# Kernel optimization log

Hardware: AMD Instinct MI355X
Metric: run time of the kernel (lower is better)

Reference implementation:

```python
import jax, jax.numpy as jnp
import numpy as np

N_CLASSES = 8  # hardcoded by the (-1, 8, 8) reshape in the original layer

def setup_inputs() -> dict:
    key = jax.random.key(0)
    k1, k2, k3, k4 = jax.random.split(key, 4)
    B, F, C, R = 16384, 128, N_CLASSES, 64
    x = jax.random.normal(k1, (B, F), dtype=jnp.float32)
    p = jax.random.uniform(k2, (B, C), dtype=jnp.float32)  # class-prob-like input
    W = jax.random.normal(k3, (F, C * C, R), dtype=jnp.float32) * 0.02
    b = jax.random.normal(k4, (C, C, R), dtype=jnp.float32) * 0.1
    return {"x": x, "p": p, "W": W, "b": b}

def reference(x, p, W, b):
    # x: (B, 128) features; p: (B, C) class probs; W: (128, C*C, R); b: (C, C, R)
    B = x.shape[0]
    C = b.shape[0]
    R = b.shape[-1]
    # per-annotator GEMM fused across all annotators: (B, C*C, R)
    logits = jnp.einsum('bf,fkr->bkr', x, W).reshape(B, C, C, R) + b[None]
    # row-softmax: softmax over the "predicted class" axis for each true class c
    M = jax.nn.softmax(logits, axis=2)  # (B, C, C, R)
    # batched dot: p (B,C) contracted against rows of each annotator matrix
    out = jnp.einsum('bc,bcdr->bdr', p, M)  # (B, C, R)
    # NOTE: original applies K.dropout(0.5) (training-mode); omitted for a
    # deterministic inference reference (identity at eval).
    return out
```

## Files before the change

kernel.cpp:

```cpp
#include <hip/hip_runtime.h>
#include <hip/hip_bf16.h>


#define B_ROWS   16384
#define F_DIM    128
#define NCOL     4096
#define OUT_STRIDE 512
#define LOG2E    1.44269504088896340736f

typedef __bf16 bf16x8 __attribute__((ext_vector_type(8)));
typedef float  f32x4  __attribute__((ext_vector_type(4)));

#define AS1(p) ((const __attribute__((address_space(1))) unsigned int*)(p))
#define AS3(p) ((__attribute__((address_space(3))) unsigned int*)(p))

template <int CTRL>
__device__ __forceinline__ float dpp_add(float s) {
    int si = __builtin_bit_cast(int, s);
    int pi = __builtin_amdgcn_update_dpp(0, si, CTRL, 0xf, 0xf, true);
    return s + __builtin_bit_cast(float, pi);
}

__device__ __forceinline__ float swz4(float v) {
    return __builtin_bit_cast(float,
        __builtin_amdgcn_ds_swizzle(__builtin_bit_cast(int, v), 0x101F));
}


__global__ void wconv_kernel(const float* __restrict__ W, __bf16* __restrict__ wf) {
    int f    = blockIdx.x * 256 + threadIdx.x;
    int lane = f & 63;
    int tkk  = f >> 6;
    int T    = tkk >> 2;
    int kk   = tkk & 3;
    int c    = T >> 5;
    int w    = (T >> 3) & 3;
    int i    = T & 7;
    int col4 = lane & 15;
    int d    = (col4 & 3) | ((col4 >> 1) & 4);
    int r    = w * 16 + i * 2 + ((col4 >> 2) & 1);
    int n    = (c * 8 + d) * 64 + r;
    int kbase = kk * 32 + (lane >> 4) * 8;
    bf16x8 frag;
    for (int j = 0; j < 8; ++j)
        frag[j] = (__bf16)W[(kbase + j) * NCOL + n];
    *(bf16x8*)(wf + f * 8) = frag;
}

__global__ void bconv_kernel(const float* __restrict__ bias, float* __restrict__ bs) {
    int t    = blockIdx.x * 256 + threadIdx.x;
    int lane = t & 63;
    int T    = t >> 6;
    int c    = T >> 5;
    int w    = (T >> 3) & 3;
    int i    = T & 7;
    int col4 = lane & 15;
    int d    = (col4 & 3) | ((col4 >> 1) & 4);
    int r    = w * 16 + i * 2 + ((col4 >> 2) & 1);
    bs[t] = bias[(c * 8 + d) * 64 + r] * LOG2E;
}

__global__ __launch_bounds__(256, 2)
void fused_kernel(const float* __restrict__ x, const float* __restrict__ p,
                  const float* __restrict__ bs, const __bf16* __restrict__ wf,
                  float* __restrict__ out) {
    __shared__ __align__(16) char lds[2][32768];

    const int lane = threadIdx.x & 63;
    const int ww   = threadIdx.x >> 6;
    const int quad = lane >> 4;
    const int l15  = lane & 15;
    const int w    = blockIdx.x & 3;
    const int b0   = (blockIdx.x >> 2) * 128 + ww * 32;
    const int d    = (l15 & 3) | ((l15 >> 1) & 4);
    const int rb   = (l15 >> 2) & 1;

    bf16x8 afr[2][4];
#pragma unroll
    for (int mt = 0; mt < 2; ++mt) {
        const float* xr = x + (b0 + mt * 16 + l15) * F_DIM + quad * 8;
#pragma unroll
        for (int kk = 0; kk < 4; ++kk) {
            float4 lo = *(const float4*)(xr + kk * 32);
            float4 hi = *(const float4*)(xr + kk * 32 + 4);
            bf16x8 f;
            f[0] = (__bf16)lo.x; f[1] = (__bf16)lo.y;
            f[2] = (__bf16)lo.z; f[3] = (__bf16)lo.w;
            f[4] = (__bf16)hi.x; f[5] = (__bf16)hi.y;
            f[6] = (__bf16)hi.z; f[7] = (__bf16)hi.w;
            afr[mt][kk] = f;
        }
    }

    auto stage = [&](int c, char* dst) {
        const __bf16* gbase = wf + (size_t)(c * 128 + w * 32) * 512 + lane * 8;
#pragma unroll
        for (int j = 0; j < 8; ++j) {
            int f = ww * 8 + j;
            __builtin_amdgcn_global_load_lds(AS1(gbase + f * 512),
                                             AS3(dst + f * 1024), 16, 0, 0);
        }
    };

    float O_all[2][8][4] = {};

    stage(0, lds[0]);

#pragma unroll 1
    for (int c = 0; c < 8; ++c) {
        __syncthreads();
        if (c < 7) stage(c + 1, lds[(c + 1) & 1]);
        const char* buf = lds[c & 1];

        float pvv[2][4];
#pragma unroll
        for (int mt = 0; mt < 2; ++mt)
#pragma unroll
            for (int jj = 0; jj < 4; ++jj)
                pvv[mt][jj] = p[(b0 + mt * 16 + quad * 4 + jj) * 8 + c];

#pragma unroll
        for (int i = 0; i < 8; ++i) {
            bf16x8 bfr[4];
#pragma unroll
            for (int kk = 0; kk < 4; ++kk)
                bfr[kk] = *(const bf16x8*)(buf + (i * 4 + kk) * 1024 + lane * 16);
            f32x4 acc0 = {0.f, 0.f, 0.f, 0.f};
            f32x4 acc1 = {0.f, 0.f, 0.f, 0.f};
#pragma unroll
            for (int kk = 0; kk < 4; ++kk) {
                acc0 = __builtin_amdgcn_mfma_f32_16x16x32_bf16(afr[0][kk], bfr[kk], acc0, 0, 0, 0);
                acc1 = __builtin_amdgcn_mfma_f32_16x16x32_bf16(afr[1][kk], bfr[kk], acc1, 0, 0, 0);
            }
            float bvl = bs[(c * 32 + w * 8 + i) * 64 + lane];
#pragma unroll
            for (int mt = 0; mt < 2; ++mt) {
                const f32x4& acc = mt ? acc1 : acc0;
#pragma unroll
                for (int jj = 0; jj < 4; ++jj) {
                    float e = __builtin_amdgcn_exp2f(
                                  __builtin_fmaf(acc[jj], LOG2E, bvl));
                    float s = dpp_add<0xB1>(e);
                    s = dpp_add<0x4E>(s);
                    s = dpp_add<0x128>(s);
                    O_all[mt][i][jj] = __builtin_fmaf(
                        e, pvv[mt][jj] * __builtin_amdgcn_rcpf(s), O_all[mt][i][jj]);
                }
            }
        }
    }

    const bool bhi = (rb != 0);
#pragma unroll
    for (int mt = 0; mt < 2; ++mt) {
#pragma unroll
        for (int jj = 0; jj < 4; ++jj) {
            float S[8];
#pragma unroll
            for (int i = 0; i < 8; ++i)
                S[i] = swz4(O_all[mt][i][jj]);
            float T[8];
#pragma unroll
            for (int m = 0; m < 8; ++m) {
                int ilo = m >> 1, ihi = 4 + (m >> 1);
                float tlo = (m & 1) ? S[ilo]             : O_all[mt][ilo][jj];
                float thi = (m & 1) ? O_all[mt][ihi][jj] : S[ihi];
                T[m] = bhi ? thi : tlo;
            }
            float* orow = out + (b0 + mt * 16 + quad * 4 + jj) * OUT_STRIDE
                              + d * 64 + w * 16 + rb * 8;
            f32x4 v0 = {T[0], T[1], T[2], T[3]};
            f32x4 v1 = {T[4], T[5], T[6], T[7]};
            *(f32x4*)(orow)     = v0;
            *(f32x4*)(orow + 4) = v1;
        }
    }
}

extern "C" void kernel_launch(void* const* d_in, const int* in_sizes, int n_in,
                              void* d_out, int out_size, void* d_ws, size_t ws_size,
                              hipStream_t stream) {
    const float* x    = (const float*)d_in[0];
    const float* p    = (const float*)d_in[1];
    const float* W    = (const float*)d_in[2];
    const float* bias = (const float*)d_in[3];
    float* out = (float*)d_out;
    __bf16* wf = (__bf16*)d_ws;
    float*  bs = (float*)((char*)d_ws + (1 << 20));

    wconv_kernel<<<dim3(256), dim3(256), 0, stream>>>(W, wf);
    bconv_kernel<<<dim3(64), dim3(256), 0, stream>>>(bias, bs);
    fused_kernel<<<dim3(512), dim3(256), 0, stream>>>(x, p, bs, wf, out);
}
```

Baseline: 114.4 us.

## Split each block's columns across two wave halves with 512-thread blocks

Doubles the block size to eight waves, with each group of four waves handling half of the per-class column tiles for the same rows. This halves accumulator registers per thread and spreads the MFMA/softmax work over more waves to raise latency hiding. The cost is duplicated x fragment loads and p loads per wave pair, and a narrower output store per lane.

```diff
diff --git a/kernel.cpp b/kernel.cpp
--- a/kernel.cpp
+++ b/kernel.cpp
@@ -60,7 +60,7 @@
     bs[t] = bias[(c * 8 + d) * 64 + r] * LOG2E;
 }
 
-__global__ __launch_bounds__(256, 2)
+__global__ __launch_bounds__(512, 4)
 void fused_kernel(const float* __restrict__ x, const float* __restrict__ p,
                   const float* __restrict__ bs, const __bf16* __restrict__ wf,
                   float* __restrict__ out) {
@@ -68,10 +68,12 @@
 
     const int lane = threadIdx.x & 63;
     const int ww   = threadIdx.x >> 6;
+    const int mtp  = ww & 3;
+    const int h    = ww >> 2;
     const int quad = lane >> 4;
     const int l15  = lane & 15;
     const int w    = blockIdx.x & 3;
-    const int b0   = (blockIdx.x >> 2) * 128 + ww * 32;
+    const int b0   = (blockIdx.x >> 2) * 128 + mtp * 32;
     const int d    = (l15 & 3) | ((l15 >> 1) & 4);
     const int rb   = (l15 >> 2) & 1;
 
@@ -95,14 +97,14 @@
     auto stage = [&](int c, char* dst) {
         const __bf16* gbase = wf + (size_t)(c * 128 + w * 32) * 512 + lane * 8;
 #pragma unroll
-        for (int j = 0; j < 8; ++j) {
-            int f = ww * 8 + j;
+        for (int j = 0; j < 4; ++j) {
+            int f = ww * 4 + j;
             __builtin_amdgcn_global_load_lds(AS1(gbase + f * 512),
                                              AS3(dst + f * 1024), 16, 0, 0);
         }
     };
 
-    float O_all[2][8][4] = {};
+    float O_all[2][4][4] = {};
 
     stage(0, lds[0]);
 
@@ -120,17 +122,15 @@
                 pvv[mt][jj] = p[(b0 + mt * 16 + quad * 4 + jj) * 8 + c];
 
 #pragma unroll
-        for (int i = 0; i < 8; ++i) {
-            bf16x8 bfr[4];
-#pragma unroll
-            for (int kk = 0; kk < 4; ++kk)
-                bfr[kk] = *(const bf16x8*)(buf + (i * 4 + kk) * 1024 + lane * 16);
+        for (int ii = 0; ii < 4; ++ii) {
+            const int i = h * 4 + ii;
             f32x4 acc0 = {0.f, 0.f, 0.f, 0.f};
             f32x4 acc1 = {0.f, 0.f, 0.f, 0.f};
 #pragma unroll
             for (int kk = 0; kk < 4; ++kk) {
-                acc0 = __builtin_amdgcn_mfma_f32_16x16x32_bf16(afr[0][kk], bfr[kk], acc0, 0, 0, 0);
-                acc1 = __builtin_amdgcn_mfma_f32_16x16x32_bf16(afr[1][kk], bfr[kk], acc1, 0, 0, 0);
+                bf16x8 bfr = *(const bf16x8*)(buf + (i * 4 + kk) * 1024 + lane * 16);
+                acc0 = __builtin_amdgcn_mfma_f32_16x16x32_bf16(afr[0][kk], bfr, acc0, 0, 0, 0);
+                acc1 = __builtin_amdgcn_mfma_f32_16x16x32_bf16(afr[1][kk], bfr, acc1, 0, 0, 0);
             }
             float bvl = bs[(c * 32 + w * 8 + i) * 64 + lane];
 #pragma unroll
@@ -143,8 +143,8 @@
                     float s = dpp_add<0xB1>(e);
                     s = dpp_add<0x4E>(s);
                     s = dpp_add<0x128>(s);
-                    O_all[mt][i][jj] = __builtin_fmaf(
-                        e, pvv[mt][jj] * __builtin_amdgcn_rcpf(s), O_all[mt][i][jj]);
+                    O_all[mt][ii][jj] = __builtin_fmaf(
+                        e, pvv[mt][jj] * __builtin_amdgcn_rcpf(s), O_all[mt][ii][jj]);
                 }
             }
         }
@@ -155,24 +155,23 @@
     for (int mt = 0; mt < 2; ++mt) {
 #pragma unroll
         for (int jj = 0; jj < 4; ++jj) {
-            float S[8];
+            float S[4];
 #pragma unroll
-            for (int i = 0; i < 8; ++i)
-                S[i] = swz4(O_all[mt][i][jj]);
-            float T[8];
+            for (int ii = 0; ii < 4; ++ii)
+                S[ii] = swz4(O_all[mt][ii][jj]);
+            float T[4];
 #pragma unroll
-            for (int m = 0; m < 8; ++m) {
-                int ilo = m >> 1, ihi = 4 + (m >> 1);
+            for (int m = 0; m < 4; ++m) {
+                int ilo = m >> 1;
+                int ihi = 2 + (m >> 1);
                 float tlo = (m & 1) ? S[ilo]             : O_all[mt][ilo][jj];
                 float thi = (m & 1) ? O_all[mt][ihi][jj] : S[ihi];
                 T[m] = bhi ? thi : tlo;
             }
             float* orow = out + (b0 + mt * 16 + quad * 4 + jj) * OUT_STRIDE
-                              + d * 64 + w * 16 + rb * 8;
-            f32x4 v0 = {T[0], T[1], T[2], T[3]};
-            f32x4 v1 = {T[4], T[5], T[6], T[7]};
-            *(f32x4*)(orow)     = v0;
-            *(f32x4*)(orow + 4) = v1;
+                              + d * 64 + w * 16 + h * 8 + rb * 4;
+            f32x4 v = {T[0], T[1], T[2], T[3]};
+            *(f32x4*)(orow) = v;
         }
     }
 }
@@ -190,5 +189,5 @@
 
     wconv_kernel<<<dim3(256), dim3(256), 0, stream>>>(W, wf);
     bconv_kernel<<<dim3(64), dim3(256), 0, stream>>>(bias, bs);
-    fused_kernel<<<dim3(512), dim3(256), 0, stream>>>(x, p, bs, wf, out);
+    fused_kernel<<<dim3(512), dim3(512), 0, stream>>>(x, p, bs, wf, out);
 }
```

New measurement: 127.0 us. 1.11x slower.
